# Kernel tuning notes

Measured on AMD Instinct MI355X. Metric: run time of the kernel, lower is better.

Reference implementation:

```python
import jax, jax.numpy as jnp
import numpy as np
from jax import lax

# --- config (matches init_kwargs) ---
H = 1024          # hidden_size
I = 704           # moe_intermediate_size (per expert)
E = 32            # n_routed_experts
G = 8             # n_group
TOPK_GROUP = 3    # topk_group
K = 6             # num_experts_per_tok
N_SHARED = 2      # n_shared_experts -> shared intermediate = N_SHARED * I
SCALE = 1.0       # routed_scaling_factor
T = 2048          # number of tokens
CAP = 2 * (T * K) // E


def setup_inputs() -> dict:
    key = jax.random.key(0)
    ks = jax.random.split(key, 8)
    s = 0.02  # initializer_range
    Is = N_SHARED * I
    return {
        "x": jax.random.normal(ks[0], (T, H), jnp.float32),
        "gate_w": s * jax.random.normal(ks[1], (E, H), jnp.float32),   # router
        "w_gate": s * jax.random.normal(ks[2], (E, H, I), jnp.float32),
        "w_up":   s * jax.random.normal(ks[3], (E, H, I), jnp.float32),
        "w_down": s * jax.random.normal(ks[4], (E, I, H), jnp.float32),
        "sw_gate": s * jax.random.normal(ks[5], (H, Is), jnp.float32),
        "sw_up":   s * jax.random.normal(ks[6], (H, Is), jnp.float32),
        "sw_down": s * jax.random.normal(ks[7], (Is, H), jnp.float32),
    }


def _moe_forward(x, gate_w, w_gate, w_up, w_down, sw_gate, sw_up, sw_down):
    # ---- router: softmax scores + group-limited top-k (topk_method='gready') ----
    logits = x @ gate_w.T                                  # [T, E]
    scores = jax.nn.softmax(logits, axis=-1)               # [T, E]
    group_scores = scores.reshape(T, G, E // G).max(-1)    # [T, G]
    _, gidx = lax.top_k(group_scores, TOPK_GROUP)          # [T, topk_group]
    gmask = jnp.zeros((T, G), scores.dtype).at[jnp.arange(T)[:, None], gidx].set(1.0)
    emask = jnp.repeat(gmask, E // G, axis=1)              # [T, E]
    masked_scores = jnp.where(emask > 0, scores, 0.0)
    topk_w, topk_idx = lax.top_k(masked_scores, K)         # [T, K]
    # norm_topk_prob=False -> weights are raw softmax scores * routed_scaling_factor
    topk_w = topk_w * SCALE

    # ---- dispatch: sort assignments by expert, scatter into [E, CAP, H] buffers ----
    flat_e = topk_idx.reshape(-1)                          # [T*K]
    order = jnp.argsort(flat_e)
    se = flat_e[order]                                     # sorted expert ids
    tok = order // K                                       # source token of each slot
    counts = jax.ops.segment_sum(jnp.ones_like(flat_e), flat_e, num_segments=E)
    starts = jnp.cumsum(counts) - counts
    pos = jnp.arange(T * K) - starts[se]                   # position within expert
    valid = pos < CAP
    pos_w = jnp.where(valid, pos, CAP)                     # overflow slot CAP (sliced off)
    xbuf = jnp.zeros((E, CAP + 1, H), x.dtype).at[se, pos_w].set(x[tok])
    xb = xbuf[:, :CAP]                                     # [E, CAP, H]

    # ---- grouped expert MLPs: silu(x Wg) * (x Wu) @ Wd ----
    g = jnp.einsum("ech,ehi->eci", xb, w_gate)
    u = jnp.einsum("ech,ehi->eci", xb, w_up)
    yb = jnp.einsum("eci,eih->ech", jax.nn.silu(g) * u, w_down)  # [E, CAP, H]

    # ---- combine: gather back and weighted-scatter to tokens ----
    y_flat = yb[se, jnp.minimum(pos, CAP - 1)] * valid[:, None].astype(x.dtype)
    wts = topk_w.reshape(-1)[order]                        # [T*K]
    routed = jnp.zeros((T, H), x.dtype).at[tok].add(y_flat * wts[:, None])

    # ---- shared experts MLP (intermediate = n_shared * moe_inter) ----
    sg = jax.nn.silu(x @ sw_gate) * (x @ sw_up)
    shared = sg @ sw_down

    return routed + shared                                 # [T, H]


def reference(x, gate_w, w_gate, w_up, w_down, sw_gate, sw_up, sw_down):
    return _moe_forward(x, gate_w, w_gate, w_up, w_down, sw_gate, sw_up, sw_down)
```

## Files before the change

### kernel.cpp

```cpp
#include <hip/hip_runtime.h>
#include <hip/hip_bf16.h>

#define H 1024
#define I_DIM 704
#define E 32
#define TOPK_GROUP 3
#define K_TOP 6
#define T_TOK 2048
#define CAP 768
#define IS_DIM 1408

typedef __attribute__((ext_vector_type(8))) short short8v;
typedef __attribute__((ext_vector_type(4))) float f32x4;

__device__ __forceinline__ unsigned short f2bfbits(float f) {
  unsigned u = __float_as_uint(f);
  unsigned r = (u + 0x7fffu + ((u >> 16) & 1u)) >> 16;
  return (unsigned short)r;
}
__device__ __forceinline__ unsigned packbf2(float lo, float hi) {
  return (unsigned)f2bfbits(lo) | ((unsigned)f2bfbits(hi) << 16);
}
__device__ __forceinline__ void gload_lds16(const short* g, short* l) {
  __builtin_amdgcn_global_load_lds(
      (const __attribute__((address_space(1))) unsigned int*)g,
      (__attribute__((address_space(3))) unsigned int*)l, 16, 0, 0);
}

__global__ void cast_x_kernel(const float* __restrict__ x, short* __restrict__ xb) {
  size_t i = ((size_t)blockIdx.x * 256 + threadIdx.x) * 4;
  float4 v = *(const float4*)(x + i);
  short4 s;
  s.x = (short)f2bfbits(v.x); s.y = (short)f2bfbits(v.y);
  s.z = (short)f2bfbits(v.z); s.w = (short)f2bfbits(v.w);
  *(short4*)(xb + i) = s;
}

__global__ __launch_bounds__(256) void transpose_cast_kernel(
    const float* __restrict__ in, short* __restrict__ outp,
    int C, int N, long long in_stride, long long out_stride) {
  int e = blockIdx.z;
  const float* src = in + (long long)e * in_stride;
  short* dst = outp + (long long)e * out_stride;
  int n0 = blockIdx.x * 64, c0 = blockIdx.y * 64;
  __shared__ unsigned ldsb[64][34];
  int t = threadIdx.x;
  int n4 = t & 15;
  int kp = t >> 4;
  #pragma unroll
  for (int p = 0; p < 2; ++p) {
    int c = c0 + p * 32 + 2 * kp;
    const float* s0 = src + (long long)c * N + n0 + 4 * n4;
    float4 a = *(const float4*)s0;
    float4 b = *(const float4*)(s0 + N);
    int cc = p * 16 + kp;
    ldsb[4 * n4 + 0][cc] = packbf2(a.x, b.x);
    ldsb[4 * n4 + 1][cc] = packbf2(a.y, b.y);
    ldsb[4 * n4 + 2][cc] = packbf2(a.z, b.z);
    ldsb[4 * n4 + 3][cc] = packbf2(a.w, b.w);
  }
  __syncthreads();
  int ch = t & 7;
  int nr = t >> 3;
  #pragma unroll
  for (int p = 0; p < 2; ++p) {
    int n = p * 32 + nr;
    uint4 v;
    v.x = ldsb[n][4 * ch + 0]; v.y = ldsb[n][4 * ch + 1];
    v.z = ldsb[n][4 * ch + 2]; v.w = ldsb[n][4 * ch + 3];
    *(uint4*)(dst + (size_t)(n0 + n) * C + c0 + 8 * ch) = v;
  }
}

__global__ __launch_bounds__(64) void gating_kernel(const float* __restrict__ x,
                                                    const float* __restrict__ gw,
                                                    int* __restrict__ tidx,
                                                    float* __restrict__ tw) {
  int t = blockIdx.x;
  int lane = threadIdx.x;
  int e = lane & 31, half = lane >> 5;
  const float* xr = x + (size_t)t * H;
  const float* wr = gw + (size_t)e * H;
  const float4* xr4 = (const float4*)(xr + half * 512);
  const float4* wr4 = (const float4*)(wr + half * 512);
  double acc = 0.0;
  #pragma unroll 4
  for (int j = 0; j < 128; ++j) {
    float4 a = xr4[j], b = wr4[j];
    acc += (double)a.x * b.x + (double)a.y * b.y + (double)a.z * b.z + (double)a.w * b.w;
  }
  acc += __shfl_down(acc, 32);
  __shared__ double sc[32];
  if (lane < 32) sc[lane] = acc;
  __syncthreads();
  if (lane == 0) {
    double p[32];
    double m = -1e300;
    for (int i = 0; i < 32; ++i) if (sc[i] > m) m = sc[i];
    double sum = 0.0;
    for (int i = 0; i < 32; ++i) { p[i] = exp(sc[i] - m); sum += p[i]; }
    for (int i = 0; i < 32; ++i) p[i] /= sum;
    double gs[8];
    for (int g = 0; g < 8; ++g) {
      double mm = p[4 * g];
      for (int j = 1; j < 4; ++j) if (p[4 * g + j] > mm) mm = p[4 * g + j];
      gs[g] = mm;
    }
    bool gsel[8] = {false,false,false,false,false,false,false,false};
    for (int it = 0; it < TOPK_GROUP; ++it) {
      int best = -1; double bv = -1e300;
      for (int g = 0; g < 8; ++g) if (!gsel[g] && gs[g] > bv) { bv = gs[g]; best = g; }
      gsel[best] = true;
    }
    double mp[32];
    for (int i = 0; i < 32; ++i) mp[i] = gsel[i >> 2] ? p[i] : 0.0;
    for (int it = 0; it < K_TOP; ++it) {
      int best = -1; double bv = -1e300;
      for (int i = 0; i < 32; ++i) if (mp[i] > bv) { bv = mp[i]; best = i; }
      tidx[t * K_TOP + it] = best;
      tw[t * K_TOP + it] = (float)bv;
      mp[best] = -2.0;
    }
  }
}

__global__ __launch_bounds__(64) void dispatch_kernel(const int* __restrict__ tidx,
                                                      const float* __restrict__ tw,
                                                      int* __restrict__ token_list,
                                                      float* __restrict__ slot_w,
                                                      int* __restrict__ cnt) {
  int e = blockIdx.x;
  int lane = threadIdx.x;
  int base = 0;
  for (int c = 0; c < T_TOK * K_TOP; c += 64) {
    int idx = c + lane;
    int te = tidx[idx];
    bool m = (te == e);
    unsigned long long bal = __ballot(m);
    if (m) {
      int pos = base + __popcll(bal & ((1ull << lane) - 1ull));
      if (pos < CAP) {
        token_list[e * CAP + pos] = idx / K_TOP;
        slot_w[e * CAP + pos] = tw[idx];
      }
    }
    base += __popcll(bal);
  }
  if (lane == 0) cnt[e] = base < CAP ? base : CAP;
}

__global__ __launch_bounds__(256) void gateup_kernel(
    const short* __restrict__ Xb, const short* __restrict__ WgT, const short* __restrict__ WuT,
    short* __restrict__ Sout, const int* __restrict__ tlist, const int* __restrict__ cnt_dev,
    int Nld, long long wstride, long long sstride) {
  int e = blockIdx.z;
  int cnt = cnt_dev ? cnt_dev[e] : T_TOK;
  int row0 = blockIdx.y * 128;
  if (row0 >= cnt) return;
  int col0 = blockIdx.x * 64;
  const short* wg = WgT + (long long)e * wstride;
  const short* wu = WuT + (long long)e * wstride;
  short* sbase = Sout + (long long)e * sstride;

  __shared__ __align__(16) short As[128 * 32];
  __shared__ __align__(16) short Bgs[64 * 32];
  __shared__ __align__(16) short Bus[64 * 32];

  int tid = threadIdx.x;
  int lane = tid & 63, wave = tid >> 6;
  int rr = tid >> 2, ch = tid & 3;

  int ra0 = row0 + rr, ra1 = ra0 + 64;
  if (tlist) {
    const int* tl = tlist + e * CAP;
    ra0 = tl[min(ra0, cnt - 1)];
    ra1 = tl[min(ra1, cnt - 1)];
  }
  const short* pa0 = Xb + (size_t)ra0 * H + ch * 8;
  const short* pa1 = Xb + (size_t)ra1 * H + ch * 8;
  const short* pbg = wg + (size_t)(col0 + rr) * H + ch * 8;
  const short* pbu = wu + (size_t)(col0 + rr) * H + ch * 8;

  short* ldsA0 = &As[(wave * 16) * 32];
  short* ldsA1 = &As[(64 + wave * 16) * 32];
  short* ldsBg = &Bgs[(wave * 16) * 32];
  short* ldsBu = &Bus[(wave * 16) * 32];

  int wm = wave & 1, wn = wave >> 1;
  int c = lane & 15, q = lane >> 4;
  const short* fA = &As[(wm * 64 + c) * 32 + q * 8];
  const short* fBg = &Bgs[(wn * 32 + c) * 32 + q * 8];
  const short* fBu = &Bus[(wn * 32 + c) * 32 + q * 8];

  f32x4 accg[4][2], accu[4][2];
  #pragma unroll
  for (int i = 0; i < 4; ++i)
    #pragma unroll
    for (int j = 0; j < 2; ++j) {
      accg[i][j] = (f32x4){0.f, 0.f, 0.f, 0.f};
      accu[i][j] = (f32x4){0.f, 0.f, 0.f, 0.f};
    }

  for (int k0 = 0; k0 < H; k0 += 32) {
    __syncthreads();
    gload_lds16(pa0 + k0, ldsA0);
    gload_lds16(pa1 + k0, ldsA1);
    gload_lds16(pbg + k0, ldsBg);
    gload_lds16(pbu + k0, ldsBu);
    __syncthreads();
    short8v a[4], bg[2], bu[2];
    #pragma unroll
    for (int mi = 0; mi < 4; ++mi) a[mi] = *(const short8v*)(fA + mi * 16 * 32);
    #pragma unroll
    for (int ni = 0; ni < 2; ++ni) {
      bg[ni] = *(const short8v*)(fBg + ni * 16 * 32);
      bu[ni] = *(const short8v*)(fBu + ni * 16 * 32);
    }
    #pragma unroll
    for (int mi = 0; mi < 4; ++mi)
      #pragma unroll
      for (int ni = 0; ni < 2; ++ni) {
        accg[mi][ni] = __builtin_amdgcn_mfma_f32_16x16x32_bf16(a[mi], bg[ni], accg[mi][ni], 0, 0, 0);
        accu[mi][ni] = __builtin_amdgcn_mfma_f32_16x16x32_bf16(a[mi], bu[ni], accu[mi][ni], 0, 0, 0);
      }
  }
  #pragma unroll
  for (int mi = 0; mi < 4; ++mi) {
    int rbase = row0 + wm * 64 + mi * 16 + q * 4;
    #pragma unroll
    for (int ni = 0; ni < 2; ++ni) {
      int col = col0 + wn * 32 + ni * 16 + c;
      #pragma unroll
      for (int r = 0; r < 4; ++r) {
        float g = accg[mi][ni][r], u = accu[mi][ni][r];
        float s = (g / (1.f + __expf(-g))) * u;
        sbase[(size_t)(rbase + r) * Nld + col] = (short)f2bfbits(s);
      }
    }
  }
}

__global__ __launch_bounds__(256) void down_kernel(
    const short* __restrict__ Sin, const short* __restrict__ WdT, float* __restrict__ out,
    const int* __restrict__ tlist, const float* __restrict__ slot_w, const int* __restrict__ cnt_dev,
    int Kdim, long long wstride, long long sstride) {
  int e = blockIdx.z;
  int cnt = cnt_dev ? cnt_dev[e] : T_TOK;
  int row0 = blockIdx.y * 128;
  if (row0 >= cnt) return;
  int col0 = blockIdx.x * 128;
  const short* sb = Sin + (long long)e * sstride;
  const short* wd = WdT + (long long)e * wstride;

  __shared__ __align__(16) short As[128 * 32];
  __shared__ __align__(16) short Bs[128 * 32];

  int tid = threadIdx.x;
  int lane = tid & 63, wave = tid >> 6;
  int rr = tid >> 2, ch = tid & 3;

  const short* pa0 = sb + (size_t)(row0 + rr) * Kdim + ch * 8;
  const short* pa1 = pa0 + (size_t)64 * Kdim;
  const short* pb0 = wd + (size_t)(col0 + rr) * Kdim + ch * 8;
  const short* pb1 = pb0 + (size_t)64 * Kdim;

  short* ldsA0 = &As[(wave * 16) * 32];
  short* ldsA1 = &As[(64 + wave * 16) * 32];
  short* ldsB0 = &Bs[(wave * 16) * 32];
  short* ldsB1 = &Bs[(64 + wave * 16) * 32];

  int wm = wave & 1, wn = wave >> 1;
  int c = lane & 15, q = lane >> 4;
  const short* fA = &As[(wm * 64 + c) * 32 + q * 8];
  const short* fB = &Bs[(wn * 64 + c) * 32 + q * 8];

  f32x4 acc[4][4];
  #pragma unroll
  for (int i = 0; i < 4; ++i)
    #pragma unroll
    for (int j = 0; j < 4; ++j) acc[i][j] = (f32x4){0.f, 0.f, 0.f, 0.f};

  for (int k0 = 0; k0 < Kdim; k0 += 32) {
    __syncthreads();
    gload_lds16(pa0 + k0, ldsA0);
    gload_lds16(pa1 + k0, ldsA1);
    gload_lds16(pb0 + k0, ldsB0);
    gload_lds16(pb1 + k0, ldsB1);
    __syncthreads();
    short8v a[4], b[4];
    #pragma unroll
    for (int mi = 0; mi < 4; ++mi) a[mi] = *(const short8v*)(fA + mi * 16 * 32);
    #pragma unroll
    for (int ni = 0; ni < 4; ++ni) b[ni] = *(const short8v*)(fB + ni * 16 * 32);
    #pragma unroll
    for (int mi = 0; mi < 4; ++mi)
      #pragma unroll
      for (int ni = 0; ni < 4; ++ni)
        acc[mi][ni] = __builtin_amdgcn_mfma_f32_16x16x32_bf16(a[mi], b[ni], acc[mi][ni], 0, 0, 0);
  }

  if (tlist) {
    const int* tl = tlist + e * CAP;
    const float* swt = slot_w + e * CAP;
    #pragma unroll
    for (int mi = 0; mi < 4; ++mi) {
      int rb = row0 + wm * 64 + mi * 16 + q * 4;
      #pragma unroll
      for (int r = 0; r < 4; ++r) {
        int s = rb + r;
        if (s < cnt) {
          int tkn = tl[s];
          float w = swt[s];
          #pragma unroll
          for (int ni = 0; ni < 4; ++ni) {
            int col = col0 + wn * 64 + ni * 16 + c;
            atomicAdd(&out[(size_t)tkn * H + col], w * acc[mi][ni][r]);
          }
        }
      }
    }
  } else {
    #pragma unroll
    for (int mi = 0; mi < 4; ++mi) {
      int rb = row0 + wm * 64 + mi * 16 + q * 4;
      #pragma unroll
      for (int ni = 0; ni < 4; ++ni) {
        int col = col0 + wn * 64 + ni * 16 + c;
        #pragma unroll
        for (int r = 0; r < 4; ++r)
          out[(size_t)(rb + r) * H + col] = acc[mi][ni][r];
      }
    }
  }
}

extern "C" void kernel_launch(void* const* d_in, const int* in_sizes, int n_in,
                              void* d_out, int out_size, void* d_ws, size_t ws_size,
                              hipStream_t stream) {
  const float* x       = (const float*)d_in[0];
  const float* gate_w  = (const float*)d_in[1];
  const float* w_gate  = (const float*)d_in[2];
  const float* w_up    = (const float*)d_in[3];
  const float* w_down  = (const float*)d_in[4];
  const float* sw_gate = (const float*)d_in[5];
  const float* sw_up   = (const float*)d_in[6];
  const float* sw_down = (const float*)d_in[7];
  float* out = (float*)d_out;
  char* ws = (char*)d_ws;

  size_t o = 0;
  short* xb   = (short*)(ws + o); o += (size_t)T_TOK * H * 2;
  short* Sr   = (short*)(ws + o); o += (size_t)E * CAP * I_DIM * 2;
  short* Ss   = (short*)(ws + o); o += (size_t)T_TOK * IS_DIM * 2;
  short* wgT  = (short*)(ws + o); o += (size_t)E * I_DIM * H * 2;
  short* wuT  = (short*)(ws + o); o += (size_t)E * I_DIM * H * 2;
  short* wdT  = (short*)(ws + o); o += (size_t)E * H * I_DIM * 2;
  short* swgT = (short*)(ws + o); o += (size_t)IS_DIM * H * 2;
  short* swuT = (short*)(ws + o); o += (size_t)IS_DIM * H * 2;
  short* swdT = (short*)(ws + o); o += (size_t)H * IS_DIM * 2;
  int*   tidx = (int*)(ws + o);   o += (size_t)T_TOK * K_TOP * 4;
  float* twt  = (float*)(ws + o); o += (size_t)T_TOK * K_TOP * 4;
  int*   tl   = (int*)(ws + o);   o += (size_t)E * CAP * 4;
  float* swt  = (float*)(ws + o); o += (size_t)E * CAP * 4;
  int*   cnt  = (int*)(ws + o);   o += 256;

  cast_x_kernel<<<(T_TOK * H) / 1024, 256, 0, stream>>>(x, xb);
  gating_kernel<<<T_TOK, 64, 0, stream>>>(x, gate_w, tidx, twt);
  dispatch_kernel<<<E, 64, 0, stream>>>(tidx, twt, tl, swt, cnt);

  transpose_cast_kernel<<<dim3(I_DIM / 64, H / 64, E), 256, 0, stream>>>(
      w_gate, wgT, H, I_DIM, (long long)H * I_DIM, (long long)I_DIM * H);
  transpose_cast_kernel<<<dim3(I_DIM / 64, H / 64, E), 256, 0, stream>>>(
      w_up, wuT, H, I_DIM, (long long)H * I_DIM, (long long)I_DIM * H);
  transpose_cast_kernel<<<dim3(H / 64, I_DIM / 64, E), 256, 0, stream>>>(
      w_down, wdT, I_DIM, H, (long long)I_DIM * H, (long long)H * I_DIM);
  transpose_cast_kernel<<<dim3(IS_DIM / 64, H / 64, 1), 256, 0, stream>>>(
      sw_gate, swgT, H, IS_DIM, 0, 0);
  transpose_cast_kernel<<<dim3(IS_DIM / 64, H / 64, 1), 256, 0, stream>>>(
      sw_up, swuT, H, IS_DIM, 0, 0);
  transpose_cast_kernel<<<dim3(H / 64, IS_DIM / 64, 1), 256, 0, stream>>>(
      sw_down, swdT, IS_DIM, H, 0, 0);

  gateup_kernel<<<dim3(I_DIM / 64, CAP / 128, E), 256, 0, stream>>>(
      xb, wgT, wuT, Sr, tl, cnt, I_DIM, (long long)I_DIM * H, (long long)CAP * I_DIM);
  gateup_kernel<<<dim3(IS_DIM / 64, T_TOK / 128, 1), 256, 0, stream>>>(
      xb, swgT, swuT, Ss, nullptr, nullptr, IS_DIM, 0, 0);
  down_kernel<<<dim3(H / 128, T_TOK / 128, 1), 256, 0, stream>>>(
      Ss, swdT, out, nullptr, nullptr, nullptr, IS_DIM, 0, 0);
  down_kernel<<<dim3(H / 128, CAP / 128, E), 256, 0, stream>>>(
      Sr, wdT, out, tl, swt, cnt, I_DIM, (long long)H * I_DIM, (long long)CAP * I_DIM);
}
```

Measured before the change: 664.2 us.

## Parallelize gating top-k with wave shuffles and split dispatch into hist/scan/place

The gating kernel's serial single-lane softmax and group/expert top-k selection are replaced with wave-wide shuffle reductions, so each of the 32 lanes holds one expert. The expert dispatch, previously 32 single-wave blocks each scanning all 12288 assignments, becomes a three-kernel chunked histogram, exclusive scan and placement pipeline. This removes serial work from the routing path at the cost of two extra kernel launches. Slot order within each expert is kept stable, and ties now break explicitly toward the lower index.

```diff
diff --git a/kernel.cpp b/kernel.cpp
--- a/kernel.cpp
+++ b/kernel.cpp
@@ -9,6 +9,7 @@
 #define T_TOK 2048
 #define CAP 768
 #define IS_DIM 1408
+#define NCHUNK 192
 
 typedef __attribute__((ext_vector_type(8))) short short8v;
 typedef __attribute__((ext_vector_type(4))) float f32x4;
@@ -79,10 +80,8 @@
   int t = blockIdx.x;
   int lane = threadIdx.x;
   int e = lane & 31, half = lane >> 5;
-  const float* xr = x + (size_t)t * H;
-  const float* wr = gw + (size_t)e * H;
-  const float4* xr4 = (const float4*)(xr + half * 512);
-  const float4* wr4 = (const float4*)(wr + half * 512);
+  const float4* xr4 = (const float4*)(x + (size_t)t * H + half * 512);
+  const float4* wr4 = (const float4*)(gw + (size_t)e * H + half * 512);
   double acc = 0.0;
   #pragma unroll 4
   for (int j = 0; j < 128; ++j) {
@@ -90,63 +89,101 @@
     acc += (double)a.x * b.x + (double)a.y * b.y + (double)a.z * b.z + (double)a.w * b.w;
   }
   acc += __shfl_down(acc, 32);
-  __shared__ double sc[32];
-  if (lane < 32) sc[lane] = acc;
+  double lg = acc;
+  double m = lg;
+  #pragma unroll
+  for (int off = 16; off >= 1; off >>= 1) {
+    double o = __shfl_xor(m, off);
+    if (o > m) m = o;
+  }
+  double p = exp(lg - m);
+  double sum = p;
+  #pragma unroll
+  for (int off = 16; off >= 1; off >>= 1) sum += __shfl_xor(sum, off);
+  p /= sum;
+  double gmax = p;
+  { double o = __shfl_xor(gmax, 1); if (o > gmax) gmax = o;
+    o = __shfl_xor(gmax, 2); if (o > gmax) gmax = o; }
+  bool gsel = false;
+  double gv = gmax;
+  #pragma unroll
+  for (int it = 0; it < TOPK_GROUP; ++it) {
+    double v = gv; int gi = e >> 2;
+    #pragma unroll
+    for (int off = 16; off >= 1; off >>= 1) {
+      double ov = __shfl_xor(v, off);
+      int oi = __shfl_xor(gi, off);
+      if (ov > v || (ov == v && oi < gi)) { v = ov; gi = oi; }
+    }
+    if ((e >> 2) == gi) { gsel = true; gv = -1e300; }
+  }
+  double mp = gsel ? p : 0.0;
+  #pragma unroll
+  for (int it = 0; it < K_TOP; ++it) {
+    double v = mp; int ei = e;
+    #pragma unroll
+    for (int off = 16; off >= 1; off >>= 1) {
+      double ov = __shfl_xor(v, off);
+      int oi = __shfl_xor(ei, off);
+      if (ov > v || (ov == v && oi < ei)) { v = ov; ei = oi; }
+    }
+    if (lane == 0) { tidx[t * K_TOP + it] = ei; tw[t * K_TOP + it] = (float)v; }
+    if (e == ei) mp = -2.0;
+  }
+}
+
+__global__ __launch_bounds__(64) void hist_kernel(const int* __restrict__ tidx,
+                                                  int* __restrict__ chunk_hist) {
+  __shared__ int h[E];
+  int c = blockIdx.x, lane = threadIdx.x;
+  if (lane < E) h[lane] = 0;
   __syncthreads();
-  if (lane == 0) {
-    double p[32];
-    double m = -1e300;
-    for (int i = 0; i < 32; ++i) if (sc[i] > m) m = sc[i];
-    double sum = 0.0;
-    for (int i = 0; i < 32; ++i) { p[i] = exp(sc[i] - m); sum += p[i]; }
-    for (int i = 0; i < 32; ++i) p[i] /= sum;
-    double gs[8];
-    for (int g = 0; g < 8; ++g) {
-      double mm = p[4 * g];
-      for (int j = 1; j < 4; ++j) if (p[4 * g + j] > mm) mm = p[4 * g + j];
-      gs[g] = mm;
-    }
-    bool gsel[8] = {false,false,false,false,false,false,false,false};
-    for (int it = 0; it < TOPK_GROUP; ++it) {
-      int best = -1; double bv = -1e300;
-      for (int g = 0; g < 8; ++g) if (!gsel[g] && gs[g] > bv) { bv = gs[g]; best = g; }
-      gsel[best] = true;
-    }
-    double mp[32];
-    for (int i = 0; i < 32; ++i) mp[i] = gsel[i >> 2] ? p[i] : 0.0;
-    for (int it = 0; it < K_TOP; ++it) {
-      int best = -1; double bv = -1e300;
-      for (int i = 0; i < 32; ++i) if (mp[i] > bv) { bv = mp[i]; best = i; }
-      tidx[t * K_TOP + it] = best;
-      tw[t * K_TOP + it] = (float)bv;
-      mp[best] = -2.0;
-    }
-  }
-}
-
-__global__ __launch_bounds__(64) void dispatch_kernel(const int* __restrict__ tidx,
-                                                      const float* __restrict__ tw,
-                                                      int* __restrict__ token_list,
-                                                      float* __restrict__ slot_w,
-                                                      int* __restrict__ cnt) {
-  int e = blockIdx.x;
-  int lane = threadIdx.x;
-  int base = 0;
-  for (int c = 0; c < T_TOK * K_TOP; c += 64) {
-    int idx = c + lane;
-    int te = tidx[idx];
-    bool m = (te == e);
-    unsigned long long bal = __ballot(m);
-    if (m) {
-      int pos = base + __popcll(bal & ((1ull << lane) - 1ull));
-      if (pos < CAP) {
-        token_list[e * CAP + pos] = idx / K_TOP;
-        slot_w[e * CAP + pos] = tw[idx];
-      }
-    }
-    base += __popcll(bal);
-  }
-  if (lane == 0) cnt[e] = base < CAP ? base : CAP;
+  int te = tidx[c * 64 + lane];
+  atomicAdd(&h[te], 1);
+  __syncthreads();
+  if (lane < E) chunk_hist[c * E + lane] = h[lane];
+}
+
+__global__ __launch_bounds__(1024) void scan_kernel(const int* __restrict__ chunk_hist,
+                                                    int* __restrict__ chunk_base,
+                                                    int* __restrict__ cnt) {
+  __shared__ int h[NCHUNK * E];
+  int t = threadIdx.x;
+  for (int i = t; i < NCHUNK * E; i += 1024) h[i] = chunk_hist[i];
+  __syncthreads();
+  if (t < E) {
+    int run = 0;
+    for (int c = 0; c < NCHUNK; ++c) {
+      int v = h[c * E + t];
+      h[c * E + t] = run;
+      run += v;
+    }
+    cnt[t] = run < CAP ? run : CAP;
+  }
+  __syncthreads();
+  for (int i = t; i < NCHUNK * E; i += 1024) chunk_base[i] = h[i];
+}
+
+__global__ __launch_bounds__(64) void place_kernel(const int* __restrict__ tidx,
+                                                   const float* __restrict__ tw,
+                                                   const int* __restrict__ chunk_base,
+                                                   int* __restrict__ token_list,
+                                                   float* __restrict__ slot_w) {
+  int c = blockIdx.x, lane = threadIdx.x;
+  int idx = c * 64 + lane;
+  int te = tidx[idx];
+  unsigned long long mymask = 0;
+  #pragma unroll
+  for (int e = 0; e < E; ++e) {
+    unsigned long long bal = __ballot(te == e);
+    if (te == e) mymask = bal;
+  }
+  int rank = __popcll(mymask & ((1ull << lane) - 1ull));
+  int pos = chunk_base[c * E + te] + rank;
+  if (pos < CAP) {
+    token_list[te * CAP + pos] = idx / K_TOP;
+    slot_w[te * CAP + pos] = tw[idx];
+  }
 }
 
 __global__ __launch_bounds__(256) void gateup_kernel(
@@ -363,10 +400,14 @@
   int*   tl   = (int*)(ws + o);   o += (size_t)E * CAP * 4;
   float* swt  = (float*)(ws + o); o += (size_t)E * CAP * 4;
   int*   cnt  = (int*)(ws + o);   o += 256;
+  int*   chist = (int*)(ws + o);  o += (size_t)NCHUNK * E * 4;
+  int*   cbase = (int*)(ws + o);  o += (size_t)NCHUNK * E * 4;
 
   cast_x_kernel<<<(T_TOK * H) / 1024, 256, 0, stream>>>(x, xb);
   gating_kernel<<<T_TOK, 64, 0, stream>>>(x, gate_w, tidx, twt);
-  dispatch_kernel<<<E, 64, 0, stream>>>(tidx, twt, tl, swt, cnt);
+  hist_kernel<<<NCHUNK, 64, 0, stream>>>(tidx, chist);
+  scan_kernel<<<1, 1024, 0, stream>>>(chist, cbase, cnt);
+  place_kernel<<<NCHUNK, 64, 0, stream>>>(tidx, twt, cbase, tl, swt);
 
   transpose_cast_kernel<<<dim3(I_DIM / 64, H / 64, E), 256, 0, stream>>>(
       w_gate, wgT, H, I_DIM, (long long)H * I_DIM, (long long)I_DIM * H);
```

After: 564.2 us. -15.1%, faster.
